# Optimization experiments

Hardware: AMD Instinct MI355X
Metric: run time of the kernel (lower is better)

Reference implementation:

```python
import jax, jax.numpy as jnp
import numpy as np

B, N, D, K, H = 32768, 17, 2, 3, 64


def _mlp_params(key, n, d_in, d_hid, d_out):
    k1, k2, k3, k4 = jax.random.split(key, 4)
    W1 = jax.random.normal(k1, (n, d_in, d_hid), jnp.float32) / np.sqrt(d_in)
    b1 = jnp.zeros((n, d_hid), jnp.float32)
    W2 = jax.random.normal(k2, (n, d_hid, d_out), jnp.float32) / np.sqrt(d_hid)
    b2 = jnp.zeros((n, d_out), jnp.float32)
    return W1, b1, W2, b2


def setup_inputs() -> dict:
    key = jax.random.key(0)
    kp, kk, kw, kb = jax.random.split(key, 4)
    pred_pts = jax.random.normal(kp, (B, N, D), jnp.float32)
    kW1, kb1, kW2, kb2 = _mlp_params(kk, N, D, H, K)            # k_nets
    wW1, wb1, wW2, wb2 = _mlp_params(kw, N, D, H, K)            # weight_nets
    bW1, bb1, bW2, bb2 = _mlp_params(kb, N, D, 2 * H, K * 2 * D)  # basis_nets
    return dict(pred_pts=pred_pts,
                kW1=kW1, kb1=kb1, kW2=kW2, kb2=kb2,
                wW1=wW1, wb1=wb1, wW2=wW2, wb2=wb2,
                bW1=bW1, bb1=bb1, bW2=bW2, bb2=bb2)


def _per_joint_mlp(x, W1, b1, W2, b2):
    # x: [B,N,D]; W1: [N,D,Hd]; W2: [N,Hd,O]
    h = jax.nn.relu(jnp.einsum('bnd,ndh->bnh', x, W1) + b1[None])
    return jnp.einsum('bnh,nho->bno', h, W2) + b2[None]


def reference(pred_pts, kW1, kb1, kW2, kb2, wW1, wb1, wW2, wb2, bW1, bb1, bW2, bb2):
    Bc, Nc, Dc = pred_pts.shape
    Kc = kW2.shape[-1]

    # k-selection head (eval mode: argmax, +1)
    k_logits = _per_joint_mlp(pred_pts, kW1, kb1, kW2, kb2)      # [B,N,K]
    k_js = jnp.argmax(k_logits, axis=-1) + 1                     # [B,N] int

    # mixture weights
    w = jax.nn.softmax(_per_joint_mlp(pred_pts, wW1, wb1, wW2, wb2), axis=-1)  # [B,N,K]

    # basis parameters: mu, sigma = exp(log_sigma)
    params = _per_joint_mlp(pred_pts, bW1, bb1, bW2, bb2).reshape(Bc, Nc, Kc, 2 * Dc)
    mu = params[..., :Dc]                                         # [B,N,K,D]
    sigma = jnp.exp(params[..., Dc:])                             # [B,N,K,D]

    # top-k selection by descending weight (indices are constants w.r.t. grad)
    idx = jnp.argsort(-w, axis=-1)                                # [B,N,K]
    mu_top = jnp.take_along_axis(mu, idx[..., None], axis=2)      # [B,N,K,D]
    sigma_top = jnp.take_along_axis(sigma, idx[..., None], axis=2)
    mask = jnp.arange(Kc)[None, None, :] < k_js[..., None]        # [B,N,K] bool

    # pack float outputs: weights + selected (mu, sigma) -> [B,N,K,1+2D]
    out = jnp.concatenate([w[..., None], mu_top, sigma_top], axis=-1)
    return out, k_js, mask
```

## Files before the change

### kernel.cpp

```cpp
#include <hip/hip_runtime.h>
#include <cmath>

#define NBATCH 32768
#define NJOINT 17
#define OUT0_ELEMS (NBATCH * NJOINT * 15)
#define KJS_OFF    OUT0_ELEMS
#define MASK_OFF   (KJS_OFF + NBATCH * NJOINT)

#define WN_STRIDE 774
#define WS_DOUBLES (NJOINT * WN_STRIDE)

__device__ __forceinline__ float sel3f(int i, float a, float b, float c) {
    return (i == 0) ? a : ((i == 1) ? b : c);
}

__global__ void cvt_weights_f64(
    const float* __restrict__ kW1, const float* __restrict__ kb1,
    const float* __restrict__ kW2, const float* __restrict__ kb2,
    const float* __restrict__ wW1, const float* __restrict__ wb1,
    const float* __restrict__ wW2, const float* __restrict__ wb2,
    double* __restrict__ dws)
{
    const int n = blockIdx.x;
    double* o = dws + (size_t)n * WN_STRIDE;
    for (int i = threadIdx.x; i < WN_STRIDE; i += blockDim.x) {
        int j = i;
        const float* W1 = kW1; const float* b1 = kb1;
        const float* W2 = kW2; const float* b2 = kb2;
        if (j >= 387) { j -= 387; W1 = wW1; b1 = wb1; W2 = wW2; b2 = wb2; }
        float v;
        if (j < 128)      v = W1[n * 128 + j];
        else if (j < 192) v = b1[n * 64 + (j - 128)];
        else if (j < 384) v = W2[n * 192 + (j - 192)];
        else              v = b2[n * 3 + (j - 384)];
        o[i] = (double)v;
    }
}

__device__ __forceinline__ void mlp32_2(
    const float* __restrict__ W1, const float* __restrict__ b1f,
    const float* __restrict__ W2f, const float* __restrict__ b2f, int n,
    float xA0, float xA1, float xB0, float xB1,
    float& lA0, float& lA1, float& lA2,
    float& lB0, float& lB1, float& lB2)
{
    const float* W1a = W1 + n * 128;
    const float* W1b = W1a + 64;
    const float* b1  = b1f + n * 64;
    const float* W2  = W2f + n * 192;
    lA0 = b2f[n * 3 + 0]; lB0 = lA0;
    lA1 = b2f[n * 3 + 1]; lB1 = lA1;
    lA2 = b2f[n * 3 + 2]; lB2 = lA2;
    #pragma unroll 4
    for (int h = 0; h < 64; ++h) {
        const float wa = W1a[h], wb = W1b[h], bb = b1[h];
        const float w0 = W2[h * 3 + 0], w1 = W2[h * 3 + 1], w2 = W2[h * 3 + 2];
        float hvA = fmaxf(fmaf(xA1, wb, fmaf(xA0, wa, bb)), 0.0f);
        float hvB = fmaxf(fmaf(xB1, wb, fmaf(xB0, wa, bb)), 0.0f);
        lA0 = fmaf(hvA, w0, lA0); lB0 = fmaf(hvB, w0, lB0);
        lA1 = fmaf(hvA, w1, lA1); lB1 = fmaf(hvB, w1, lB1);
        lA2 = fmaf(hvA, w2, lA2); lB2 = fmaf(hvB, w2, lB2);
    }
}

__device__ __forceinline__ void mlp64_ws_1(
    const double* __restrict__ gws, double x0, double x1,
    double& l0, double& l1, double& l2)
{
    const double* W1a = gws;
    const double* W1b = gws + 64;
    const double* b1  = gws + 128;
    const double* W2  = gws + 192;
    l0 = gws[384]; l1 = gws[385]; l2 = gws[386];
    #pragma unroll 4
    for (int h = 0; h < 64; ++h) {
        double hv = fmax(fma(x1, W1b[h], fma(x0, W1a[h], b1[h])), 0.0);
        l0 = fma(hv, W2[h * 3 + 0], l0);
        l1 = fma(hv, W2[h * 3 + 1], l1);
        l2 = fma(hv, W2[h * 3 + 2], l2);
    }
}

__device__ __forceinline__ void mlp64_cvt_1(
    const float* __restrict__ W1, const float* __restrict__ b1f,
    const float* __restrict__ W2f, const float* __restrict__ b2f, int n,
    double x0, double x1, double& l0, double& l1, double& l2)
{
    const float* W1a = W1 + n * 128;
    const float* W1b = W1a + 64;
    const float* b1  = b1f + n * 64;
    const float* W2  = W2f + n * 192;
    l0 = (double)b2f[n * 3 + 0];
    l1 = (double)b2f[n * 3 + 1];
    l2 = (double)b2f[n * 3 + 2];
    #pragma unroll 4
    for (int h = 0; h < 64; ++h) {
        double hv = fma(x1, (double)W1b[h], fma(x0, (double)W1a[h], (double)b1[h]));
        hv = fmax(hv, 0.0);
        l0 = fma(hv, (double)W2[h * 3 + 0], l0);
        l1 = fma(hv, (double)W2[h * 3 + 1], l1);
        l2 = fma(hv, (double)W2[h * 3 + 2], l2);
    }
}

__device__ __forceinline__ bool tight3(float a, float b, float c) {
    const float m01 = fabsf(a - b), m02 = fabsf(a - c), m12 = fabsf(b - c);
    const float mn = fminf(m01, fminf(m02, m12));
    const float tau = 2e-5f * (1.0f + 0.05f * (fabsf(a) + fabsf(b) + fabsf(c)));
    return mn < tau;
}

__device__ __forceinline__ void decide(
    double kl0, double kl1, double kl2,
    double wl0, double wl1, double wl2,
    int& kj, int& i0, int& i1, int& i2,
    float& p0, float& p1, float& p2)
{
    kj = 0;
    {
        double m = kl0;
        if (kl1 > m) { m = kl1; kj = 1; }
        if (kl2 > m) { kj = 2; }
    }
    i0 = 0;
    {
        double m = wl0;
        if (wl1 > m) { m = wl1; i0 = 1; }
        if (wl2 > m) { i0 = 2; }
    }
    const int ia = (i0 == 0) ? 1 : 0;
    const int ib = (i0 == 2) ? 1 : 2;
    const double wa = ia ? wl1 : wl0;
    const double wb = (ib == 1) ? wl1 : wl2;
    i1 = (wb > wa) ? ib : ia;
    i2 = (wb > wa) ? ia : ib;

    const double mw = fmax(fmax(wl0, wl1), wl2);
    const float e0 = __expf((float)(wl0 - mw));
    const float e1 = __expf((float)(wl1 - mw));
    const float e2 = __expf((float)(wl2 - mw));
    const float inv = 1.0f / (e0 + e1 + e2);
    p0 = e0 * inv; p1 = e1 * inv; p2 = e2 * inv;
}

__device__ __forceinline__ void epilogue(
    const float acc[12], int i0, int i1, int i2,
    float p0, float p1, float p2, float r[15])
{
    r[0]  = p0; r[5] = p1; r[10] = p2;
    r[1]  = sel3f(i0, acc[0], acc[4], acc[8]);
    r[2]  = sel3f(i0, acc[1], acc[5], acc[9]);
    r[3]  = __expf(sel3f(i0, acc[2], acc[6], acc[10]));
    r[4]  = __expf(sel3f(i0, acc[3], acc[7], acc[11]));
    r[6]  = sel3f(i1, acc[0], acc[4], acc[8]);
    r[7]  = sel3f(i1, acc[1], acc[5], acc[9]);
    r[8]  = __expf(sel3f(i1, acc[2], acc[6], acc[10]));
    r[9]  = __expf(sel3f(i1, acc[3], acc[7], acc[11]));
    r[11] = sel3f(i2, acc[0], acc[4], acc[8]);
    r[12] = sel3f(i2, acc[1], acc[5], acc[9]);
    r[13] = __expf(sel3f(i2, acc[2], acc[6], acc[10]));
    r[14] = __expf(sel3f(i2, acc[3], acc[7], acc[11]));
}

template<bool USE_WS>
__device__ __forceinline__ void compute2(
    int n, float xA0f, float xA1f, float xB0f, float xB1f,
    const float* __restrict__ kW1, const float* __restrict__ kb1,
    const float* __restrict__ kW2, const float* __restrict__ kb2,
    const float* __restrict__ wW1, const float* __restrict__ wb1,
    const float* __restrict__ wW2, const float* __restrict__ wb2,
    const float* __restrict__ bW1, const float* __restrict__ bb1,
    const float* __restrict__ bW2, const float* __restrict__ bb2,
    const double* __restrict__ dws,
    float rA[15], float rB[15], int& kjA, int& kjB)
{
    float kA0, kA1, kA2, kB0, kB1, kB2;
    float wA0, wA1, wA2, wB0, wB1, wB2;
    mlp32_2(kW1, kb1, kW2, kb2, n, xA0f, xA1f, xB0f, xB1f,
            kA0, kA1, kA2, kB0, kB1, kB2);
    mlp32_2(wW1, wb1, wW2, wb2, n, xA0f, xA1f, xB0f, xB1f,
            wA0, wA1, wA2, wB0, wB1, wB2);

    const bool fA = tight3(kA0, kA1, kA2) || tight3(wA0, wA1, wA2);
    const bool fB = tight3(kB0, kB1, kB2) || tight3(wB0, wB1, wB2);

    double klA0 = kA0, klA1 = kA1, klA2 = kA2;
    double klB0 = kB0, klB1 = kB1, klB2 = kB2;
    double wlA0 = wA0, wlA1 = wA1, wlA2 = wA2;
    double wlB0 = wB0, wlB1 = wB1, wlB2 = wB2;

    if (__any(fA || fB)) {
        if constexpr (USE_WS) {
            const double* Wn = dws + (size_t)n * WN_STRIDE;
            if (fA) {
                mlp64_ws_1(Wn,       (double)xA0f, (double)xA1f, klA0, klA1, klA2);
                mlp64_ws_1(Wn + 387, (double)xA0f, (double)xA1f, wlA0, wlA1, wlA2);
            }
            if (fB) {
                mlp64_ws_1(Wn,       (double)xB0f, (double)xB1f, klB0, klB1, klB2);
                mlp64_ws_1(Wn + 387, (double)xB0f, (double)xB1f, wlB0, wlB1, wlB2);
            }
        } else {
            if (fA) {
                mlp64_cvt_1(kW1, kb1, kW2, kb2, n, (double)xA0f, (double)xA1f, klA0, klA1, klA2);
                mlp64_cvt_1(wW1, wb1, wW2, wb2, n, (double)xA0f, (double)xA1f, wlA0, wlA1, wlA2);
            }
            if (fB) {
                mlp64_cvt_1(kW1, kb1, kW2, kb2, n, (double)xB0f, (double)xB1f, klB0, klB1, klB2);
                mlp64_cvt_1(wW1, wb1, wW2, wb2, n, (double)xB0f, (double)xB1f, wlB0, wlB1, wlB2);
            }
        }
    }

    int i0A, i1A, i2A, i0B, i1B, i2B;
    float p0A, p1A, p2A, p0B, p1B, p2B;
    decide(klA0, klA1, klA2, wlA0, wlA1, wlA2, kjA, i0A, i1A, i2A, p0A, p1A, p2A);
    decide(klB0, klB1, klB2, wlB0, wlB1, wlB2, kjB, i0B, i1B, i2B, p0B, p1B, p2B);

    float accA[12], accB[12];
    {
        const float* W1a = bW1 + n * 256;
        const float* W1b = W1a + 128;
        const float* b1  = bb1 + n * 128;
        const float* W2  = bW2 + n * 1536;
        const float* b2  = bb2 + n * 12;
        #pragma unroll
        for (int j = 0; j < 12; ++j) { accA[j] = b2[j]; accB[j] = b2[j]; }
        #pragma unroll 4
        for (int h = 0; h < 128; ++h) {
            const float wa = W1a[h], wb = W1b[h], bb = b1[h];
            float hvA = fmaxf(fmaf(xA1f, wb, fmaf(xA0f, wa, bb)), 0.0f);
            float hvB = fmaxf(fmaf(xB1f, wb, fmaf(xB0f, wa, bb)), 0.0f);
            #pragma unroll
            for (int j = 0; j < 12; ++j) {
                const float wv = W2[h * 12 + j];
                accA[j] = fmaf(hvA, wv, accA[j]);
                accB[j] = fmaf(hvB, wv, accB[j]);
            }
        }
    }

    epilogue(accA, i0A, i1A, i2A, p0A, p1A, p2A, rA);
    epilogue(accB, i0B, i1B, i2B, p0B, p1B, p2B, rB);
}

template<bool USE_WS>
__global__ __launch_bounds__(128, 4) void mdn_fused(
    const float* __restrict__ pred_pts,
    const float* __restrict__ kW1, const float* __restrict__ kb1,
    const float* __restrict__ kW2, const float* __restrict__ kb2,
    const float* __restrict__ wW1, const float* __restrict__ wb1,
    const float* __restrict__ wW2, const float* __restrict__ wb2,
    const float* __restrict__ bW1, const float* __restrict__ bb1,
    const float* __restrict__ bW2, const float* __restrict__ bb2,
    float* __restrict__ out,
    const double* __restrict__ dws)
{
    const int l    = threadIdx.x;
    const int w    = l >> 6;
    const int lane = l & 63;
    const int bx   = blockIdx.x;
    const int by   = blockIdx.y;
    const int n0   = by * 2;

    if (by == 8 && w == 1) return;
    int n = n0 + w;
    n = __builtin_amdgcn_readfirstlane(n);

    const int bA = bx * 128 + lane;
    const int bB = bA + 64;
    const int pA = bA * NJOINT + n;
    const int pB = bB * NJOINT + n;

    const float2 xA = *reinterpret_cast<const float2*>(pred_pts + 2 * pA);
    const float2 xB = *reinterpret_cast<const float2*>(pred_pts + 2 * pB);

    float rA[15], rB[15];
    int kjA, kjB;
    compute2<USE_WS>(n, xA.x, xA.y, xB.x, xB.y,
                     kW1, kb1, kW2, kb2, wW1, wb1, wW2, wb2,
                     bW1, bb1, bW2, bb2, dws, rA, rB, kjA, kjB);

    if (by == 8) {
        float* oA = out + (size_t)pA * 15;
        float* oB = out + (size_t)pB * 15;
        #pragma unroll
        for (int i = 0; i < 15; ++i) { oA[i] = rA[i]; oB[i] = rB[i]; }
        out[KJS_OFF + pA] = (float)(kjA + 1);
        out[KJS_OFF + pB] = (float)(kjB + 1);
        float* mkA = out + MASK_OFF + (size_t)pA * 3;
        mkA[0] = 1.0f; mkA[1] = (kjA >= 1) ? 1.0f : 0.0f; mkA[2] = (kjA >= 2) ? 1.0f : 0.0f;
        float* mkB = out + MASK_OFF + (size_t)pB * 3;
        mkB[0] = 1.0f; mkB[1] = (kjB >= 1) ? 1.0f : 0.0f; mkB[2] = (kjB >= 2) ? 1.0f : 0.0f;
        return;
    }

    __shared__ float s_out[256 * 17];
    {
        float* soA = s_out + (w * 128 + lane) * 17;
        float* soB = soA + 64 * 17;
        #pragma unroll
        for (int j = 0; j < 15; ++j) { soA[j] = rA[j]; soB[j] = rB[j]; }
        soA[15] = (float)(kjA + 1);
        soB[15] = (float)(kjB + 1);
    }
    __syncthreads();

    if (l < 120) {
        const int c_off = l / 30;
        const int jj    = l - c_off * 30;
        const int nl    = jj / 15;
        const int j     = jj - nl * 15;
        const int lbase = (nl * 128 + c_off) * 17 + j;
        size_t g = (size_t)((bx * 128 + c_off) * NJOINT + n0) * 15 + jj;
        #pragma unroll
        for (int rr = 0; rr < 32; ++rr) {
            out[g] = s_out[lbase + 68 * rr];
            g += 1020;
        }
    }

    #pragma unroll
    for (int it = 0; it < 2; ++it) {
        const int q   = it * 128 + l;
        const int bl  = q >> 1;
        const int nlr = q & 1;
        const float kjf = s_out[(nlr * 128 + bl) * 17 + 15];
        const int pg = (bx * 128 + bl) * NJOINT + n0 + nlr;
        out[KJS_OFF + pg] = kjf;
        float* mk = out + MASK_OFF + (size_t)pg * 3;
        mk[0] = 1.0f;
        mk[1] = (kjf >= 1.5f) ? 1.0f : 0.0f;
        mk[2] = (kjf >= 2.5f) ? 1.0f : 0.0f;
    }
}

extern "C" void kernel_launch(void* const* d_in, const int* in_sizes, int n_in,
                              void* d_out, int out_size, void* d_ws, size_t ws_size,
                              hipStream_t stream) {
    (void)in_sizes; (void)n_in; (void)out_size;
    const bool use_ws = (d_ws != nullptr) && (ws_size >= (size_t)WS_DOUBLES * sizeof(double));
    dim3 grid(NBATCH / 128, 9);
    if (use_ws) {
        cvt_weights_f64<<<NJOINT, 256, 0, stream>>>(
            (const float*)d_in[1], (const float*)d_in[2],
            (const float*)d_in[3], (const float*)d_in[4],
            (const float*)d_in[5], (const float*)d_in[6],
            (const float*)d_in[7], (const float*)d_in[8],
            (double*)d_ws);
        mdn_fused<true><<<grid, 128, 0, stream>>>(
            (const float*)d_in[0],
            (const float*)d_in[1], (const float*)d_in[2],
            (const float*)d_in[3], (const float*)d_in[4],
            (const float*)d_in[5], (const float*)d_in[6],
            (const float*)d_in[7], (const float*)d_in[8],
            (const float*)d_in[9], (const float*)d_in[10],
            (const float*)d_in[11], (const float*)d_in[12],
            (float*)d_out, (const double*)d_ws);
    } else {
        mdn_fused<false><<<grid, 128, 0, stream>>>(
            (const float*)d_in[0],
            (const float*)d_in[1], (const float*)d_in[2],
            (const float*)d_in[3], (const float*)d_in[4],
            (const float*)d_in[5], (const float*)d_in[6],
            (const float*)d_in[7], (const float*)d_in[8],
            (const float*)d_in[9], (const float*)d_in[10],
            (const float*)d_in[11], (const float*)d_in[12],
            (float*)d_out, nullptr);
    }
}
```

Before: 145.6 us.

## Split fused MDN kernel into selection and basis kernels via global intermediate

Splits the single fused kernel into two. The first computes the k and weight heads, with an fp64 fallback for near-tie cases, and writes the softmax probabilities and packed argmax/sort indices to a global float4 buffer. The second computes the basis MLP and epilogue from that buffer. The aim is to lower register pressure per kernel and separate the divergent fp64 path from the dense basis MLP. The cost is an extra launch and a round trip through global memory for the intermediate.

```diff
diff --git a/kernel.cpp b/kernel.cpp
--- a/kernel.cpp
+++ b/kernel.cpp
@@ -9,6 +9,8 @@
 
 #define WN_STRIDE 774
 #define WS_DOUBLES (NJOINT * WN_STRIDE)
+
+__device__ __align__(16) float4 g_inter[NBATCH * NJOINT];
 
 __device__ __forceinline__ float sel3f(int i, float a, float b, float c) {
     return (i == 0) ? a : ((i == 1) ? b : c);
@@ -163,22 +165,38 @@
 }
 
 template<bool USE_WS>
-__device__ __forceinline__ void compute2(
-    int n, float xA0f, float xA1f, float xB0f, float xB1f,
+__global__ __launch_bounds__(128, 4) void mdn_kw(
+    const float* __restrict__ pred_pts,
     const float* __restrict__ kW1, const float* __restrict__ kb1,
     const float* __restrict__ kW2, const float* __restrict__ kb2,
     const float* __restrict__ wW1, const float* __restrict__ wb1,
     const float* __restrict__ wW2, const float* __restrict__ wb2,
-    const float* __restrict__ bW1, const float* __restrict__ bb1,
-    const float* __restrict__ bW2, const float* __restrict__ bb2,
-    const double* __restrict__ dws,
-    float rA[15], float rB[15], int& kjA, int& kjB)
-{
+    const double* __restrict__ dws)
+{
+    const int l    = threadIdx.x;
+    const int w    = l >> 6;
+    const int lane = l & 63;
+    const int bx   = blockIdx.x;
+    const int by   = blockIdx.y;
+    const int n0   = by * 2;
+
+    if (by == 8 && w == 1) return;
+    int n = n0 + w;
+    n = __builtin_amdgcn_readfirstlane(n);
+
+    const int bA = bx * 128 + lane;
+    const int bB = bA + 64;
+    const int pA = bA * NJOINT + n;
+    const int pB = bB * NJOINT + n;
+
+    const float2 xA = *reinterpret_cast<const float2*>(pred_pts + 2 * pA);
+    const float2 xB = *reinterpret_cast<const float2*>(pred_pts + 2 * pB);
+
     float kA0, kA1, kA2, kB0, kB1, kB2;
     float wA0, wA1, wA2, wB0, wB1, wB2;
-    mlp32_2(kW1, kb1, kW2, kb2, n, xA0f, xA1f, xB0f, xB1f,
+    mlp32_2(kW1, kb1, kW2, kb2, n, xA.x, xA.y, xB.x, xB.y,
             kA0, kA1, kA2, kB0, kB1, kB2);
-    mlp32_2(wW1, wb1, wW2, wb2, n, xA0f, xA1f, xB0f, xB1f,
+    mlp32_2(wW1, wb1, wW2, wb2, n, xA.x, xA.y, xB.x, xB.y,
             wA0, wA1, wA2, wB0, wB1, wB2);
 
     const bool fA = tight3(kA0, kA1, kA2) || tight3(wA0, wA1, wA2);
@@ -193,29 +211,67 @@
         if constexpr (USE_WS) {
             const double* Wn = dws + (size_t)n * WN_STRIDE;
             if (fA) {
-                mlp64_ws_1(Wn,       (double)xA0f, (double)xA1f, klA0, klA1, klA2);
-                mlp64_ws_1(Wn + 387, (double)xA0f, (double)xA1f, wlA0, wlA1, wlA2);
+                mlp64_ws_1(Wn,       (double)xA.x, (double)xA.y, klA0, klA1, klA2);
+                mlp64_ws_1(Wn + 387, (double)xA.x, (double)xA.y, wlA0, wlA1, wlA2);
             }
             if (fB) {
-                mlp64_ws_1(Wn,       (double)xB0f, (double)xB1f, klB0, klB1, klB2);
-                mlp64_ws_1(Wn + 387, (double)xB0f, (double)xB1f, wlB0, wlB1, wlB2);
+                mlp64_ws_1(Wn,       (double)xB.x, (double)xB.y, klB0, klB1, klB2);
+                mlp64_ws_1(Wn + 387, (double)xB.x, (double)xB.y, wlB0, wlB1, wlB2);
             }
         } else {
             if (fA) {
-                mlp64_cvt_1(kW1, kb1, kW2, kb2, n, (double)xA0f, (double)xA1f, klA0, klA1, klA2);
-                mlp64_cvt_1(wW1, wb1, wW2, wb2, n, (double)xA0f, (double)xA1f, wlA0, wlA1, wlA2);
+                mlp64_cvt_1(kW1, kb1, kW2, kb2, n, (double)xA.x, (double)xA.y, klA0, klA1, klA2);
+                mlp64_cvt_1(wW1, wb1, wW2, wb2, n, (double)xA.x, (double)xA.y, wlA0, wlA1, wlA2);
             }
             if (fB) {
-                mlp64_cvt_1(kW1, kb1, kW2, kb2, n, (double)xB0f, (double)xB1f, klB0, klB1, klB2);
-                mlp64_cvt_1(wW1, wb1, wW2, wb2, n, (double)xB0f, (double)xB1f, wlB0, wlB1, wlB2);
+                mlp64_cvt_1(kW1, kb1, kW2, kb2, n, (double)xB.x, (double)xB.y, klB0, klB1, klB2);
+                mlp64_cvt_1(wW1, wb1, wW2, wb2, n, (double)xB.x, (double)xB.y, wlB0, wlB1, wlB2);
             }
         }
     }
 
-    int i0A, i1A, i2A, i0B, i1B, i2B;
+    int kjA, i0A, i1A, i2A, kjB, i0B, i1B, i2B;
     float p0A, p1A, p2A, p0B, p1B, p2B;
     decide(klA0, klA1, klA2, wlA0, wlA1, wlA2, kjA, i0A, i1A, i2A, p0A, p1A, p2A);
     decide(klB0, klB1, klB2, wlB0, wlB1, wlB2, kjB, i0B, i1B, i2B, p0B, p1B, p2B);
+
+    const int packA = kjA | (i0A << 2) | (i1A << 4) | (i2A << 6);
+    const int packB = kjB | (i0B << 2) | (i1B << 4) | (i2B << 6);
+    g_inter[n * NBATCH + bA] = make_float4(p0A, p1A, p2A, __int_as_float(packA));
+    g_inter[n * NBATCH + bB] = make_float4(p0B, p1B, p2B, __int_as_float(packB));
+}
+
+__global__ __launch_bounds__(128, 4) void mdn_b(
+    const float* __restrict__ pred_pts,
+    const float* __restrict__ bW1, const float* __restrict__ bb1,
+    const float* __restrict__ bW2, const float* __restrict__ bb2,
+    float* __restrict__ out)
+{
+    const int l    = threadIdx.x;
+    const int w    = l >> 6;
+    const int lane = l & 63;
+    const int bx   = blockIdx.x;
+    const int by   = blockIdx.y;
+    const int n0   = by * 2;
+
+    if (by == 8 && w == 1) return;
+    int n = n0 + w;
+    n = __builtin_amdgcn_readfirstlane(n);
+
+    const int bA = bx * 128 + lane;
+    const int bB = bA + 64;
+    const int pA = bA * NJOINT + n;
+    const int pB = bB * NJOINT + n;
+
+    const float2 xA = *reinterpret_cast<const float2*>(pred_pts + 2 * pA);
+    const float2 xB = *reinterpret_cast<const float2*>(pred_pts + 2 * pB);
+
+    const float4 qA = g_inter[n * NBATCH + bA];
+    const float4 qB = g_inter[n * NBATCH + bB];
+    const int packA = __float_as_int(qA.w);
+    const int packB = __float_as_int(qB.w);
+    const int kjA = packA & 3, i0A = (packA >> 2) & 3, i1A = (packA >> 4) & 3, i2A = (packA >> 6) & 3;
+    const int kjB = packB & 3, i0B = (packB >> 2) & 3, i1B = (packB >> 4) & 3, i2B = (packB >> 6) & 3;
 
     float accA[12], accB[12];
     {
@@ -229,8 +285,8 @@
         #pragma unroll 4
         for (int h = 0; h < 128; ++h) {
             const float wa = W1a[h], wb = W1b[h], bb = b1[h];
-            float hvA = fmaxf(fmaf(xA1f, wb, fmaf(xA0f, wa, bb)), 0.0f);
-            float hvB = fmaxf(fmaf(xB1f, wb, fmaf(xB0f, wa, bb)), 0.0f);
+            float hvA = fmaxf(fmaf(xA.y, wb, fmaf(xA.x, wa, bb)), 0.0f);
+            float hvB = fmaxf(fmaf(xB.y, wb, fmaf(xB.x, wa, bb)), 0.0f);
             #pragma unroll
             for (int j = 0; j < 12; ++j) {
                 const float wv = W2[h * 12 + j];
@@ -240,46 +296,9 @@
         }
     }
 
-    epilogue(accA, i0A, i1A, i2A, p0A, p1A, p2A, rA);
-    epilogue(accB, i0B, i1B, i2B, p0B, p1B, p2B, rB);
-}
-
-template<bool USE_WS>
-__global__ __launch_bounds__(128, 4) void mdn_fused(
-    const float* __restrict__ pred_pts,
-    const float* __restrict__ kW1, const float* __restrict__ kb1,
-    const float* __restrict__ kW2, const float* __restrict__ kb2,
-    const float* __restrict__ wW1, const float* __restrict__ wb1,
-    const float* __restrict__ wW2, const float* __restrict__ wb2,
-    const float* __restrict__ bW1, const float* __restrict__ bb1,
-    const float* __restrict__ bW2, const float* __restrict__ bb2,
-    float* __restrict__ out,
-    const double* __restrict__ dws)
-{
-    const int l    = threadIdx.x;
-    const int w    = l >> 6;
-    const int lane = l & 63;
-    const int bx   = blockIdx.x;
-    const int by   = blockIdx.y;
-    const int n0   = by * 2;
-
-    if (by == 8 && w == 1) return;
-    int n = n0 + w;
-    n = __builtin_amdgcn_readfirstlane(n);
-
-    const int bA = bx * 128 + lane;
-    const int bB = bA + 64;
-    const int pA = bA * NJOINT + n;
-    const int pB = bB * NJOINT + n;
-
-    const float2 xA = *reinterpret_cast<const float2*>(pred_pts + 2 * pA);
-    const float2 xB = *reinterpret_cast<const float2*>(pred_pts + 2 * pB);
-
     float rA[15], rB[15];
-    int kjA, kjB;
-    compute2<USE_WS>(n, xA.x, xA.y, xB.x, xB.y,
-                     kW1, kb1, kW2, kb2, wW1, wb1, wW2, wb2,
-                     bW1, bb1, bW2, bb2, dws, rA, rB, kjA, kjB);
+    epilogue(accA, i0A, i1A, i2A, qA.x, qA.y, qA.z, rA);
+    epilogue(accB, i0B, i1B, i2B, qB.x, qB.y, qB.z, rB);
 
     if (by == 8) {
         float* oA = out + (size_t)pA * 15;
@@ -341,6 +360,7 @@
     (void)in_sizes; (void)n_in; (void)out_size;
     const bool use_ws = (d_ws != nullptr) && (ws_size >= (size_t)WS_DOUBLES * sizeof(double));
     dim3 grid(NBATCH / 128, 9);
+
     if (use_ws) {
         cvt_weights_f64<<<NJOINT, 256, 0, stream>>>(
             (const float*)d_in[1], (const float*)d_in[2],
@@ -348,24 +368,26 @@
             (const float*)d_in[5], (const float*)d_in[6],
             (const float*)d_in[7], (const float*)d_in[8],
             (double*)d_ws);
-        mdn_fused<true><<<grid, 128, 0, stream>>>(
+        mdn_kw<true><<<grid, 128, 0, stream>>>(
             (const float*)d_in[0],
             (const float*)d_in[1], (const float*)d_in[2],
             (const float*)d_in[3], (const float*)d_in[4],
             (const float*)d_in[5], (const float*)d_in[6],
             (const float*)d_in[7], (const float*)d_in[8],
-            (const float*)d_in[9], (const float*)d_in[10],
-            (const float*)d_in[11], (const float*)d_in[12],
-            (float*)d_out, (const double*)d_ws);
+            (const double*)d_ws);
     } else {
-        mdn_fused<false><<<grid, 128, 0, stream>>>(
+        mdn_kw<false><<<grid, 128, 0, stream>>>(
             (const float*)d_in[0],
             (const float*)d_in[1], (const float*)d_in[2],
             (const float*)d_in[3], (const float*)d_in[4],
             (const float*)d_in[5], (const float*)d_in[6],
             (const float*)d_in[7], (const float*)d_in[8],
-            (const float*)d_in[9], (const float*)d_in[10],
-            (const float*)d_in[11], (const float*)d_in[12],
-            (float*)d_out, nullptr);
-    }
-}
+            nullptr);
+    }
+
+    mdn_b<<<grid, 128, 0, stream>>>(
+        (const float*)d_in[0],
+        (const float*)d_in[9], (const float*)d_in[10],
+        (const float*)d_in[11], (const float*)d_in[12],
+        (float*)d_out);
+}
```

Result: slower. 155.0 us (+6.5%).
